# Kernel tuning notes

Measured on AMD Instinct MI355X. Metric: run time of the kernel, lower is better.

Reference implementation:

```python
import jax, jax.numpy as jnp
import numpy as np

B, S, H, K, L, NH, FF = 4, 2048, 2048, 1024, 2, 16, 4096
EPS = 1e-5

def _alibi_slopes(n):
    # standard power-of-two ALiBi slopes
    start = 2.0 ** (-8.0 / n)
    return start ** jnp.arange(1, n + 1, dtype=jnp.float32)

def _layernorm(h, g, b):
    mu = jnp.mean(h, axis=-1, keepdims=True)
    var = jnp.mean(jnp.square(h - mu), axis=-1, keepdims=True)
    return (h - mu) * jax.lax.rsqrt(var + EPS) * g + b

def setup_inputs() -> dict:
    key = jax.random.key(0)
    ks = jax.random.split(key, 16)
    x = jax.random.normal(ks[0], (B, S, H), jnp.float32)
    prev = jax.random.normal(ks[1], (B, S, H), jnp.float32)
    # unique sorted token indices per batch row (jit-friendly boolean mask)
    idx = jnp.stack([jnp.sort(jax.random.permutation(jax.random.fold_in(ks[2], b), S)[:K])
                     for b in range(B)]).astype(jnp.int32)
    w = 0.02
    Wq = jax.random.normal(ks[3], (L, H, H), jnp.float32) * w
    Wk = jax.random.normal(ks[4], (L, H, H), jnp.float32) * w
    Wv = jax.random.normal(ks[5], (L, H, H), jnp.float32) * w
    Wo = jax.random.normal(ks[6], (L, H, H), jnp.float32) * w
    attn_gamma = jnp.ones((L, H), jnp.float32)
    attn_beta = jnp.zeros((L, H), jnp.float32)
    mlp_gamma = jnp.ones((L, H), jnp.float32)
    mlp_beta = jnp.zeros((L, H), jnp.float32)
    Wgate = jax.random.normal(ks[7], (L, H, FF), jnp.float32) * w
    Wup = jax.random.normal(ks[8], (L, H, FF), jnp.float32) * w
    Wdown = jax.random.normal(ks[9], (L, FF, H), jnp.float32) * w
    return {"x": x, "prev": prev, "idx": idx, "Wq": Wq, "Wk": Wk, "Wv": Wv,
            "Wo": Wo, "attn_gamma": attn_gamma, "attn_beta": attn_beta,
            "mlp_gamma": mlp_gamma, "mlp_beta": mlp_beta,
            "Wgate": Wgate, "Wup": Wup, "Wdown": Wdown}

def _forward(x, prev, idx, Wq, Wk, Wv, Wo, attn_gamma, attn_beta,
             mlp_gamma, mlp_beta, Wgate, Wup, Wdown):
    d = H // NH
    scale = 1.0 / jnp.sqrt(jnp.asarray(d, jnp.float32))
    # gather selected tokens: [B, K, H]
    cur = jnp.take_along_axis(x, idx[:, :, None], axis=1)
    mem = jnp.take_along_axis(prev, idx[:, :, None], axis=1)
    # non-causal ALiBi bias over selected-sequence positions: [NH, K, K]
    pos = jnp.arange(K)
    dist = jnp.abs(pos[:, None] - pos[None, :]).astype(jnp.float32)
    bias = -_alibi_slopes(NH)[:, None, None] * dist
    for l in range(L):
        q = (cur @ Wq[l]).reshape(B, K, NH, d)
        k = (mem @ Wk[l]).reshape(B, K, NH, d)
        v = (mem @ Wv[l]).reshape(B, K, NH, d)
        scores = jnp.einsum('bqhd,bkhd->bhqk', q, k) * scale + bias
        attn = jax.nn.softmax(scores, axis=-1)
        o = jnp.einsum('bhqk,bkhd->bqhd', attn, v).reshape(B, K, H) @ Wo[l]
        cur = cur + o
        normed = _layernorm(cur, attn_gamma[l], attn_beta[l])
        mlp = (jax.nn.silu(normed @ Wgate[l]) * (normed @ Wup[l])) @ Wdown[l]
        cur = cur + mlp
        cur = _layernorm(cur, mlp_gamma[l], mlp_beta[l])
    # scatter-add back: out[mask] += update_val
    out = x.at[jnp.arange(B)[:, None], idx].add(cur)
    return out

def reference(x, prev, idx, Wq, Wk, Wv, Wo, attn_gamma, attn_beta,
              mlp_gamma, mlp_beta, Wgate, Wup, Wdown):
    return _forward(x, prev, idx, Wq, Wk, Wv, Wo, attn_gamma, attn_beta,
                    mlp_gamma, mlp_beta, Wgate, Wup, Wdown)
```

## Files before the change

### kernel.cpp

```cpp
#include <hip/hip_runtime.h>
#include <hip/hip_bf16.h>

#define BB 4
#define SS 2048
#define HH 2048
#define KK 1024
#define LL 2
#define NHH 16
#define FFF 4096
#define DD 128

typedef __attribute__((ext_vector_type(8))) short s8v;
typedef __attribute__((ext_vector_type(4))) short s4v;
typedef __attribute__((ext_vector_type(4))) float f4v;

__device__ __forceinline__ short f2bf(float f) {
  unsigned u = __builtin_bit_cast(unsigned, f);
  u += 0x7fffu + ((u >> 16) & 1u);
  return (short)(u >> 16);
}
__device__ __forceinline__ float bf2f(short s) {
  unsigned u = ((unsigned)(unsigned short)s) << 16;
  return __builtin_bit_cast(float, u);
}
__device__ __forceinline__ f4v mfma_bf16(s8v a, s8v b, f4v c) {
  asm("v_mfma_f32_16x16x32_bf16 %0, %1, %2, %0" : "+v"(c) : "v"(a), "v"(b));
  return c;
}
__device__ __forceinline__ void gload_lds16(const void* g, void* l) {
  __builtin_amdgcn_global_load_lds(
      (__attribute__((address_space(1))) void*)g,
      (__attribute__((address_space(3))) void*)l, 16, 0, 0);
}

__global__ __launch_bounds__(256) void wconv(const float* __restrict__ W,
                                             short* __restrict__ Wt,
                                             int Kd, int N) {
  __shared__ short tile[64][65];
  int n0 = blockIdx.x * 64, k0 = blockIdx.y * 64;
  int t = threadIdx.x;
#pragma unroll
  for (int i = 0; i < 16; ++i) {
    int lin = i * 256 + t;
    int r = lin >> 6, c = lin & 63;
    tile[c][r] = f2bf(W[(size_t)(k0 + r) * N + n0 + c]);
  }
  __syncthreads();
#pragma unroll
  for (int i = 0; i < 16; ++i) {
    int lin = i * 256 + t;
    int r = lin >> 6, c = lin & 63;
    Wt[(size_t)(n0 + r) * Kd + k0 + c] = tile[r][c];
  }
}

__global__ __launch_bounds__(256) void gather_rows(
    const float* __restrict__ x, const float* __restrict__ prev,
    const int* __restrict__ idx, float* __restrict__ cur_f,
    short* __restrict__ cur_b, short* __restrict__ mem_b) {
  int r = blockIdx.x;
  int b = r >> 10, kk = r & (KK - 1);
  int src = idx[b * KK + kk];
  const float4* xs = (const float4*)(x + ((size_t)b * SS + src) * HH);
  const float4* ps = (const float4*)(prev + ((size_t)b * SS + src) * HH);
  float4* cf = (float4*)(cur_f + (size_t)r * HH);
  s4v* cb = (s4v*)(cur_b + (size_t)r * HH);
  s4v* mb = (s4v*)(mem_b + (size_t)r * HH);
  int t = threadIdx.x;
#pragma unroll
  for (int i = 0; i < 2; ++i) {
    int c = t + i * 256;
    float4 xv = xs[c], pv = ps[c];
    cf[c] = xv;
    s4v cv, mv;
    cv[0] = f2bf(xv.x); cv[1] = f2bf(xv.y); cv[2] = f2bf(xv.z); cv[3] = f2bf(xv.w);
    mv[0] = f2bf(pv.x); mv[1] = f2bf(pv.y); mv[2] = f2bf(pv.z); mv[3] = f2bf(pv.w);
    cb[c] = cv; mb[c] = mv;
  }
}

template <int EPI>
__global__ __launch_bounds__(256, 2) void gemm_bt(
    const short* __restrict__ A, const short* __restrict__ Bt,
    float* __restrict__ Cf, short* __restrict__ Cb,
    const short* __restrict__ Other, int M, int N, int Kd) {
  __shared__ __align__(16) short As[128 * 32];
  __shared__ __align__(16) short Bs[128 * 32];
  int t = threadIdx.x;
  int w = t >> 6, l = t & 63;
  int wr = w >> 1, wc = w & 1;
  int l15 = l & 15, lh = l >> 4;
  int rowBase = blockIdx.y * 128, colBase = blockIdx.x * 128;

  f4v acc[4][4];
#pragma unroll
  for (int i = 0; i < 4; ++i)
#pragma unroll
    for (int j = 0; j < 4; ++j) acc[i][j] = (f4v){0.f, 0.f, 0.f, 0.f};

  int ar = t >> 2, ac = (t & 3) * 8;
  const short* gA = A + (size_t)(rowBase + ar) * Kd + ac;
  const short* gB = Bt + (size_t)(colBase + ar) * Kd + ac;
  short* lA = &As[t * 8];
  short* lB = &Bs[t * 8];
  int koff = lh * 8;

  for (int k0 = 0; k0 < Kd; k0 += 32) {
    gload_lds16(gA + k0, lA);
    gload_lds16(gA + k0 + (size_t)64 * Kd, lA + 2048);
    gload_lds16(gB + k0, lB);
    gload_lds16(gB + k0 + (size_t)64 * Kd, lB + 2048);
    __syncthreads();
    s8v af[4], bf[4];
#pragma unroll
    for (int mt = 0; mt < 4; ++mt)
      af[mt] = *(const s8v*)&As[(wr * 64 + mt * 16 + l15) * 32 + koff];
#pragma unroll
    for (int nt = 0; nt < 4; ++nt)
      bf[nt] = *(const s8v*)&Bs[(wc * 64 + nt * 16 + l15) * 32 + koff];
#pragma unroll
    for (int mt = 0; mt < 4; ++mt)
#pragma unroll
      for (int nt = 0; nt < 4; ++nt)
        acc[mt][nt] = mfma_bf16(af[mt], bf[nt], acc[mt][nt]);
    __syncthreads();
  }

#pragma unroll
  for (int mt = 0; mt < 4; ++mt) {
#pragma unroll
    for (int nt = 0; nt < 4; ++nt) {
#pragma unroll
      for (int r = 0; r < 4; ++r) {
        int row = rowBase + wr * 64 + mt * 16 + lh * 4 + r;
        int col = colBase + wc * 64 + nt * 16 + l15;
        float v = acc[mt][nt][r];
        if constexpr (EPI == 0) {
          Cb[(size_t)row * N + col] = f2bf(v);
        } else if constexpr (EPI == 1) {
          Cf[(size_t)row * N + col] += v;
        } else if constexpr (EPI == 2) {
          int b = row >> 10, ktok = row & (KK - 1);
          int h = col >> 7, dd = col & (DD - 1);
          Cb[(((size_t)(b * NHH + h)) * DD + dd) * KK + ktok] = f2bf(v);
        } else if constexpr (EPI == 3) {
          float sv = v / (1.f + __expf(-v));
          Cb[(size_t)row * N + col] = f2bf(sv);
        } else {
          float o = bf2f(Other[(size_t)row * N + col]);
          Cb[(size_t)row * N + col] = f2bf(v * o);
        }
      }
    }
  }
}

__global__ __launch_bounds__(256, 2) void attn_fwd(
    const short* __restrict__ qb, const short* __restrict__ kb,
    const short* __restrict__ vT, short* __restrict__ ob) {
  __shared__ __align__(16) short Kl[64 * 136];
  __shared__ __align__(16) short Vl[128 * 72];
  __shared__ __align__(16) short Pl[64 * 72];
  int b = blockIdx.z, h = blockIdx.y, qt = blockIdx.x;
  int t = threadIdx.x, w = t >> 6, l = t & 63, l15 = l & 15, lh = l >> 4;
  float slope = exp2f(-0.5f * (float)(h + 1));
  const float scale = 0.08838834764831845f;

  s8v qf[4];
  int qrowA = qt * 64 + w * 16 + l15;
  const short* qptr = qb + ((size_t)(b * KK + qrowA)) * HH + h * DD + lh * 8;
#pragma unroll
  for (int ks = 0; ks < 4; ++ks) qf[ks] = *(const s8v*)(qptr + ks * 32);

  f4v oacc[8];
#pragma unroll
  for (int i = 0; i < 8; ++i) oacc[i] = (f4v){0.f, 0.f, 0.f, 0.f};
  float m[4], sden[4];
#pragma unroll
  for (int r = 0; r < 4; ++r) { m[r] = -1e30f; sden[r] = 0.f; }
  int qpos_base = qt * 64 + w * 16 + lh * 4;

  for (int kt = 0; kt < KK / 64; ++kt) {
    {
      int rr = t >> 4, cc = (t & 15) * 8;
#pragma unroll
      for (int it = 0; it < 4; ++it) {
        int krow = it * 16 + rr;
        s8v g = *(const s8v*)(kb + ((size_t)(b * KK + kt * 64 + krow)) * HH + h * DD + cc);
        *(s8v*)&Kl[krow * 136 + cc] = g;
      }
      int dr = t >> 3, c2 = (t & 7) * 8;
#pragma unroll
      for (int it = 0; it < 4; ++it) {
        int drow = it * 32 + dr;
        s8v g = *(const s8v*)(vT + (((size_t)(b * NHH + h)) * DD + drow) * KK + kt * 64 + c2);
        *(s8v*)&Vl[drow * 72 + c2] = g;
      }
    }
    __syncthreads();

    f4v sacc[4];
#pragma unroll
    for (int ct = 0; ct < 4; ++ct) sacc[ct] = (f4v){0.f, 0.f, 0.f, 0.f};
#pragma unroll
    for (int ct = 0; ct < 4; ++ct)
#pragma unroll
      for (int ks = 0; ks < 4; ++ks) {
        s8v kf = *(const s8v*)&Kl[(ct * 16 + l15) * 136 + ks * 32 + lh * 8];
        sacc[ct] = mfma_bf16(qf[ks], kf, sacc[ct]);
      }

#pragma unroll
    for (int r = 0; r < 4; ++r) {
      int qpos = qpos_base + r;
      float mx = -1e30f;
#pragma unroll
      for (int ct = 0; ct < 4; ++ct) {
        int kpos = kt * 64 + ct * 16 + l15;
        float sv = sacc[ct][r] * scale - slope * fabsf((float)(qpos - kpos));
        sacc[ct][r] = sv;
        mx = fmaxf(mx, sv);
      }
      mx = fmaxf(mx, __shfl_xor(mx, 1));
      mx = fmaxf(mx, __shfl_xor(mx, 2));
      mx = fmaxf(mx, __shfl_xor(mx, 4));
      mx = fmaxf(mx, __shfl_xor(mx, 8));
      float mn = fmaxf(m[r], mx);
      float corr = __expf(m[r] - mn);
      m[r] = mn;
      float ps = 0.f;
#pragma unroll
      for (int ct = 0; ct < 4; ++ct) {
        float p = __expf(sacc[ct][r] - mn);
        sacc[ct][r] = p;
        ps += p;
      }
      ps += __shfl_xor(ps, 1); ps += __shfl_xor(ps, 2);
      ps += __shfl_xor(ps, 4); ps += __shfl_xor(ps, 8);
      sden[r] = sden[r] * corr + ps;
#pragma unroll
      for (int dt = 0; dt < 8; ++dt) oacc[dt][r] *= corr;
#pragma unroll
      for (int ct = 0; ct < 4; ++ct)
        Pl[(w * 16 + lh * 4 + r) * 72 + ct * 16 + l15] = f2bf(sacc[ct][r]);
    }

#pragma unroll
    for (int ks2 = 0; ks2 < 2; ++ks2) {
      s8v pa = *(const s8v*)&Pl[(w * 16 + l15) * 72 + ks2 * 32 + lh * 8];
#pragma unroll
      for (int dt = 0; dt < 8; ++dt) {
        s8v vf = *(const s8v*)&Vl[(dt * 16 + l15) * 72 + ks2 * 32 + lh * 8];
        oacc[dt] = mfma_bf16(pa, vf, oacc[dt]);
      }
    }
    __syncthreads();
  }

#pragma unroll
  for (int dt = 0; dt < 8; ++dt)
#pragma unroll
    for (int r = 0; r < 4; ++r) {
      int qpos = qpos_base + r;
      int dd = dt * 16 + l15;
      ob[((size_t)(b * KK + qpos)) * HH + h * DD + dd] = f2bf(oacc[dt][r] / sden[r]);
    }
}

__global__ __launch_bounds__(256) void ln_rows(const float* in,
    const float* __restrict__ gma, const float* __restrict__ bta,
    short* __restrict__ outb, float* outf) {
  __shared__ float red[2][4];
  int r = blockIdx.x, t = threadIdx.x;
  const float4* x4 = (const float4*)(in + (size_t)r * HH);
  float4 va = x4[t], vb = x4[t + 256];
  float sum = va.x + va.y + va.z + va.w + vb.x + vb.y + vb.z + vb.w;
  float sq = va.x * va.x + va.y * va.y + va.z * va.z + va.w * va.w +
             vb.x * vb.x + vb.y * vb.y + vb.z * vb.z + vb.w * vb.w;
#pragma unroll
  for (int off = 32; off; off >>= 1) {
    sum += __shfl_down(sum, off);
    sq += __shfl_down(sq, off);
  }
  int w = t >> 6;
  if ((t & 63) == 0) { red[0][w] = sum; red[1][w] = sq; }
  __syncthreads();
  sum = red[0][0] + red[0][1] + red[0][2] + red[0][3];
  sq = red[1][0] + red[1][1] + red[1][2] + red[1][3];
  float mu = sum * (1.f / HH);
  float rs = rsqrtf(sq * (1.f / HH) - mu * mu + 1e-5f);
  const float4* g4 = (const float4*)gma;
  const float4* b4 = (const float4*)bta;
  s4v* ob = (s4v*)(outb + (size_t)r * HH);
  float4* of = (float4*)(outf ? outf + (size_t)r * HH : nullptr);
#pragma unroll
  for (int i = 0; i < 2; ++i) {
    int c = t + i * 256;
    float4 v = (i == 0) ? va : vb;
    float4 g = g4[c], bb = b4[c];
    float4 nv;
    nv.x = (v.x - mu) * rs * g.x + bb.x;
    nv.y = (v.y - mu) * rs * g.y + bb.y;
    nv.z = (v.z - mu) * rs * g.z + bb.z;
    nv.w = (v.w - mu) * rs * g.w + bb.w;
    s4v o;
    o[0] = f2bf(nv.x); o[1] = f2bf(nv.y); o[2] = f2bf(nv.z); o[3] = f2bf(nv.w);
    ob[c] = o;
    if (outf) of[c] = nv;
  }
}

__global__ __launch_bounds__(256) void copy_out(const float* __restrict__ x,
                                                float* __restrict__ out, size_t n4) {
  size_t i = (size_t)blockIdx.x * 256 + threadIdx.x;
  size_t stride = (size_t)gridDim.x * 256;
  const float4* xi = (const float4*)x;
  float4* oi = (float4*)out;
  for (; i < n4; i += stride) oi[i] = xi[i];
}

__global__ __launch_bounds__(256) void scatter_add(const int* __restrict__ idx,
                                                   const float* __restrict__ cur,
                                                   float* out) {
  int r = blockIdx.x;
  int b = r >> 10, kk = r & (KK - 1);
  int dst = idx[b * KK + kk];
  float4* o = (float4*)(out + ((size_t)b * SS + dst) * HH);
  const float4* c = (const float4*)(cur + (size_t)r * HH);
  int t = threadIdx.x;
#pragma unroll
  for (int i = 0; i < 2; ++i) {
    int j = t + i * 256;
    float4 ov = o[j], cv = c[j];
    ov.x += cv.x; ov.y += cv.y; ov.z += cv.z; ov.w += cv.w;
    o[j] = ov;
  }
}

extern "C" void kernel_launch(void* const* d_in, const int* in_sizes, int n_in,
                              void* d_out, int out_size, void* d_ws, size_t ws_size,
                              hipStream_t stream) {
  (void)in_sizes; (void)n_in; (void)out_size; (void)ws_size;
  const float* x = (const float*)d_in[0];
  const float* prv = (const float*)d_in[1];
  const int* idx = (const int*)d_in[2];
  const float* Wq = (const float*)d_in[3];
  const float* Wk = (const float*)d_in[4];
  const float* Wv = (const float*)d_in[5];
  const float* Wo = (const float*)d_in[6];
  const float* ag = (const float*)d_in[7];
  const float* ab = (const float*)d_in[8];
  const float* mg = (const float*)d_in[9];
  const float* mbt = (const float*)d_in[10];
  const float* Wg = (const float*)d_in[11];
  const float* Wu = (const float*)d_in[12];
  const float* Wd = (const float*)d_in[13];
  float* out = (float*)d_out;

  char* ws = (char*)d_ws;
  size_t off = 0;
  auto alloc = [&](size_t bytes) -> void* {
    void* p = ws + off;
    off += (bytes + 255) & ~(size_t)255;
    return p;
  };
  const size_t WHH = (size_t)HH * HH, WHF = (size_t)HH * FFF;
  short* WqT = (short*)alloc(LL * WHH * 2);
  short* WkT = (short*)alloc(LL * WHH * 2);
  short* WvT = (short*)alloc(LL * WHH * 2);
  short* WoT = (short*)alloc(LL * WHH * 2);
  short* WgT = (short*)alloc(LL * WHF * 2);
  short* WuT = (short*)alloc(LL * WHF * 2);
  short* WdT = (short*)alloc(LL * WHF * 2);
  const size_t RH = (size_t)BB * KK * HH;
  float* cur_f = (float*)alloc(RH * 4);
  short* q_b = (short*)alloc(RH * 2);
  short* k_b = (short*)alloc(RH * 2);
  short* vT_b = (short*)alloc(RH * 2);
  short* o_b = (short*)alloc(RH * 2);
  short* cur_b = (short*)alloc(RH * 2);
  short* mem_b = (short*)alloc(RH * 2);
  short* nrm_b = (short*)alloc(RH * 2);
  short* sg_b = q_b;
  short* hid_b = vT_b;

  dim3 blk(256);
  for (int l = 0; l < LL; ++l) {
    wconv<<<dim3(HH / 64, HH / 64), blk, 0, stream>>>(Wq + l * WHH, WqT + l * WHH, HH, HH);
    wconv<<<dim3(HH / 64, HH / 64), blk, 0, stream>>>(Wk + l * WHH, WkT + l * WHH, HH, HH);
    wconv<<<dim3(HH / 64, HH / 64), blk, 0, stream>>>(Wv + l * WHH, WvT + l * WHH, HH, HH);
    wconv<<<dim3(HH / 64, HH / 64), blk, 0, stream>>>(Wo + l * WHH, WoT + l * WHH, HH, HH);
    wconv<<<dim3(FFF / 64, HH / 64), blk, 0, stream>>>(Wg + l * WHF, WgT + l * WHF, HH, FFF);
    wconv<<<dim3(FFF / 64, HH / 64), blk, 0, stream>>>(Wu + l * WHF, WuT + l * WHF, HH, FFF);
    wconv<<<dim3(HH / 64, FFF / 64), blk, 0, stream>>>(Wd + l * WHF, WdT + l * WHF, FFF, HH);
  }
  gather_rows<<<dim3(BB * KK), blk, 0, stream>>>(x, prv, idx, cur_f, cur_b, mem_b);

  const int M = BB * KK;
  for (int l = 0; l < LL; ++l) {
    const short* wq = WqT + l * WHH;
    const short* wk = WkT + l * WHH;
    const short* wv = WvT + l * WHH;
    const short* wo = WoT + l * WHH;
    const short* wg = WgT + l * WHF;
    const short* wu = WuT + l * WHF;
    const short* wd = WdT + l * WHF;
    gemm_bt<0><<<dim3(HH / 128, M / 128), blk, 0, stream>>>(cur_b, wq, nullptr, q_b, nullptr, M, HH, HH);
    gemm_bt<0><<<dim3(HH / 128, M / 128), blk, 0, stream>>>(mem_b, wk, nullptr, k_b, nullptr, M, HH, HH);
    gemm_bt<2><<<dim3(HH / 128, M / 128), blk, 0, stream>>>(mem_b, wv, nullptr, vT_b, nullptr, M, HH, HH);
    attn_fwd<<<dim3(KK / 64, NHH, BB), blk, 0, stream>>>(q_b, k_b, vT_b, o_b);
    gemm_bt<1><<<dim3(HH / 128, M / 128), blk, 0, stream>>>(o_b, wo, cur_f, nullptr, nullptr, M, HH, HH);
    ln_rows<<<dim3(M), blk, 0, stream>>>(cur_f, ag + l * HH, ab + l * HH, nrm_b, nullptr);
    gemm_bt<3><<<dim3(FFF / 128, M / 128), blk, 0, stream>>>(nrm_b, wg, nullptr, sg_b, nullptr, M, FFF, HH);
    gemm_bt<4><<<dim3(FFF / 128, M / 128), blk, 0, stream>>>(nrm_b, wu, nullptr, hid_b, sg_b, M, FFF, HH);
    gemm_bt<1><<<dim3(HH / 128, M / 128), blk, 0, stream>>>(hid_b, wd, cur_f, nullptr, nullptr, M, HH, FFF);
    ln_rows<<<dim3(M), blk, 0, stream>>>(cur_f, mg + l * HH, mbt + l * HH, cur_b, cur_f);
  }
  copy_out<<<dim3(2048), blk, 0, stream>>>(x, out, (size_t)BB * SS * HH / 4);
  scatter_add<<<dim3(M), blk, 0, stream>>>(idx, cur_f, out);
}
```

Before: 1.464 ms.

## Double-buffer GEMM LDS tiles with 512-thread 128x256 blocks and swizzled block order

Replaces the 256-thread 128x128 GEMM with a 512-thread kernel computing 128x256 tiles. LDS is double-buffered so the next K-slice loads while MFMAs run on the current one, leaving one barrier per iteration instead of two. Block IDs are remapped across 8 groups, likely to spread or localise work across XCDs for cache reuse. The remap assumes gridDim.y is a power of two and the block count is divisible by 8, and the larger LDS footprint may limit occupancy.

```diff
diff --git a/kernel.cpp b/kernel.cpp
--- a/kernel.cpp
+++ b/kernel.cpp
@@ -23,7 +23,7 @@
   unsigned u = ((unsigned)(unsigned short)s) << 16;
   return __builtin_bit_cast(float, u);
 }
-__device__ __forceinline__ f4v mfma_bf16(s8v a, s8v b, f4v c) {
+__device__ __forceinline__ f4v mfma16(s8v a, s8v b, f4v c) {
   asm("v_mfma_f32_16x16x32_bf16 %0, %1, %2, %0" : "+v"(c) : "v"(a), "v"(b));
   return c;
 }
@@ -80,17 +80,31 @@
 }
 
 template <int EPI>
-__global__ __launch_bounds__(256, 2) void gemm_bt(
+__global__ __launch_bounds__(512, 2) void g8p(
     const short* __restrict__ A, const short* __restrict__ Bt,
     float* __restrict__ Cf, short* __restrict__ Cb,
     const short* __restrict__ Other, int M, int N, int Kd) {
-  __shared__ __align__(16) short As[128 * 32];
-  __shared__ __align__(16) short Bs[128 * 32];
-  int t = threadIdx.x;
-  int w = t >> 6, l = t & 63;
-  int wr = w >> 1, wc = w & 1;
-  int l15 = l & 15, lh = l >> 4;
-  int rowBase = blockIdx.y * 128, colBase = blockIdx.x * 128;
+  __shared__ __align__(16) short smem[2 * 12288];
+  const int t = threadIdx.x;
+  const int w = t >> 6, l = t & 63;
+  const int wr = w >> 2, wc = w & 3;
+  const int l15 = l & 15, lh = l >> 4;
+  const int koff = lh * 8;
+
+  const int gx = gridDim.x, gy = gridDim.y;
+  const int nwg = gx * gy;
+  const int bid = blockIdx.y * gx + blockIdx.x;
+  const int wg = (bid & 7) * (nwg >> 3) + (bid >> 3);
+  const int by = wg & (gy - 1);
+  const int bx = wg / gy;
+  const int rowBase = by * 128, colBase = bx * 256;
+
+  const int ar = t >> 2, ac = (t & 3) * 8;
+  const short* gA = A + (size_t)(rowBase + ar) * Kd + ac;
+  const short* gB0 = Bt + (size_t)(colBase + ar) * Kd + ac;
+  const short* gB1 = gB0 + (size_t)128 * Kd;
+  short* lA = smem + t * 8;
+  short* lB = smem + 4096 + t * 8;
 
   f4v acc[4][4];
 #pragma unroll
@@ -98,32 +112,34 @@
 #pragma unroll
     for (int j = 0; j < 4; ++j) acc[i][j] = (f4v){0.f, 0.f, 0.f, 0.f};
 
-  int ar = t >> 2, ac = (t & 3) * 8;
-  const short* gA = A + (size_t)(rowBase + ar) * Kd + ac;
-  const short* gB = Bt + (size_t)(colBase + ar) * Kd + ac;
-  short* lA = &As[t * 8];
-  short* lB = &Bs[t * 8];
-  int koff = lh * 8;
-
-  for (int k0 = 0; k0 < Kd; k0 += 32) {
-    gload_lds16(gA + k0, lA);
-    gload_lds16(gA + k0 + (size_t)64 * Kd, lA + 2048);
-    gload_lds16(gB + k0, lB);
-    gload_lds16(gB + k0 + (size_t)64 * Kd, lB + 2048);
+  const int NT = Kd >> 5;
+  gload_lds16(gA, lA);
+  gload_lds16(gB0, lB);
+  gload_lds16(gB1, lB + 4096);
+  __syncthreads();
+
+  for (int kt = 0; kt < NT; ++kt) {
+    const short* sb = smem + (kt & 1) * 12288;
+    if (kt + 1 < NT) {
+      const int k0 = (kt + 1) * 32;
+      const int o = ((kt & 1) ^ 1) * 12288;
+      gload_lds16(gA + k0, lA + o);
+      gload_lds16(gB0 + k0, lB + o);
+      gload_lds16(gB1 + k0, lB + o + 4096);
+    }
+    s8v af[4], bf[4];
+#pragma unroll
+    for (int mt = 0; mt < 4; ++mt)
+      af[mt] = *(const s8v*)(sb + (wr * 64 + mt * 16 + l15) * 32 + koff);
+#pragma unroll
+    for (int nt = 0; nt < 4; ++nt)
+      bf[nt] = *(const s8v*)(sb + 4096 + (wc * 64 + nt * 16 + l15) * 32 + koff);
+#pragma unroll
+    for (int mt = 0; mt < 4; ++mt)
+#pragma unroll
+      for (int nt = 0; nt < 4; ++nt)
+        acc[mt][nt] = mfma16(af[mt], bf[nt], acc[mt][nt]);
     __syncthreads();
-    s8v af[4], bf[4];
-#pragma unroll
-    for (int mt = 0; mt < 4; ++mt)
-      af[mt] = *(const s8v*)&As[(wr * 64 + mt * 16 + l15) * 32 + koff];
-#pragma unroll
-    for (int nt = 0; nt < 4; ++nt)
-      bf[nt] = *(const s8v*)&Bs[(wc * 64 + nt * 16 + l15) * 32 + koff];
-#pragma unroll
-    for (int mt = 0; mt < 4; ++mt)
-#pragma unroll
-      for (int nt = 0; nt < 4; ++nt)
-        acc[mt][nt] = mfma_bf16(af[mt], bf[nt], acc[mt][nt]);
-    __syncthreads();
   }
 
 #pragma unroll
@@ -131,10 +147,10 @@
 #pragma unroll
     for (int nt = 0; nt < 4; ++nt) {
 #pragma unroll
-      for (int r = 0; r < 4; ++r) {
-        int row = rowBase + wr * 64 + mt * 16 + lh * 4 + r;
+      for (int rr = 0; rr < 4; ++rr) {
+        int row = rowBase + wr * 64 + mt * 16 + lh * 4 + rr;
         int col = colBase + wc * 64 + nt * 16 + l15;
-        float v = acc[mt][nt][r];
+        float v = acc[mt][nt][rr];
         if constexpr (EPI == 0) {
           Cb[(size_t)row * N + col] = f2bf(v);
         } else if constexpr (EPI == 1) {
@@ -207,7 +223,7 @@
 #pragma unroll
       for (int ks = 0; ks < 4; ++ks) {
         s8v kf = *(const s8v*)&Kl[(ct * 16 + l15) * 136 + ks * 32 + lh * 8];
-        sacc[ct] = mfma_bf16(qf[ks], kf, sacc[ct]);
+        sacc[ct] = mfma16(qf[ks], kf, sacc[ct]);
       }
 
 #pragma unroll
@@ -251,7 +267,7 @@
 #pragma unroll
       for (int dt = 0; dt < 8; ++dt) {
         s8v vf = *(const s8v*)&Vl[(dt * 16 + l15) * 72 + ks2 * 32 + lh * 8];
-        oacc[dt] = mfma_bf16(pa, vf, oacc[dt]);
+        oacc[dt] = mfma16(pa, vf, oacc[dt]);
       }
     }
     __syncthreads();
@@ -384,7 +400,7 @@
   short* sg_b = q_b;
   short* hid_b = vT_b;
 
-  dim3 blk(256);
+  dim3 blk(256), blk512(512);
   for (int l = 0; l < LL; ++l) {
     wconv<<<dim3(HH / 64, HH / 64), blk, 0, stream>>>(Wq + l * WHH, WqT + l * WHH, HH, HH);
     wconv<<<dim3(HH / 64, HH / 64), blk, 0, stream>>>(Wk + l * WHH, WkT + l * WHH, HH, HH);
@@ -402,18 +418,18 @@
     const short* wk = WkT + l * WHH;
     const short* wv = WvT + l * WHH;
     const short* wo = WoT + l * WHH;
-    const short* wg = WgT + l * WHF;
+    const short* wg_ = WgT + l * WHF;
     const short* wu = WuT + l * WHF;
     const short* wd = WdT + l * WHF;
-    gemm_bt<0><<<dim3(HH / 128, M / 128), blk, 0, stream>>>(cur_b, wq, nullptr, q_b, nullptr, M, HH, HH);
-    gemm_bt<0><<<dim3(HH / 128, M / 128), blk, 0, stream>>>(mem_b, wk, nullptr, k_b, nullptr, M, HH, HH);
-    gemm_bt<2><<<dim3(HH / 128, M / 128), blk, 0, stream>>>(mem_b, wv, nullptr, vT_b, nullptr, M, HH, HH);
+    g8p<0><<<dim3(HH / 256, M / 128), blk512, 0, stream>>>(cur_b, wq, nullptr, q_b, nullptr, M, HH, HH);
+    g8p<0><<<dim3(HH / 256, M / 128), blk512, 0, stream>>>(mem_b, wk, nullptr, k_b, nullptr, M, HH, HH);
+    g8p<2><<<dim3(HH / 256, M / 128), blk512, 0, stream>>>(mem_b, wv, nullptr, vT_b, nullptr, M, HH, HH);
     attn_fwd<<<dim3(KK / 64, NHH, BB), blk, 0, stream>>>(q_b, k_b, vT_b, o_b);
-    gemm_bt<1><<<dim3(HH / 128, M / 128), blk, 0, stream>>>(o_b, wo, cur_f, nullptr, nullptr, M, HH, HH);
+    g8p<1><<<dim3(HH / 256, M / 128), blk512, 0, stream>>>(o_b, wo, cur_f, nullptr, nullptr, M, HH, HH);
     ln_rows<<<dim3(M), blk, 0, stream>>>(cur_f, ag + l * HH, ab + l * HH, nrm_b, nullptr);
-    gemm_bt<3><<<dim3(FFF / 128, M / 128), blk, 0, stream>>>(nrm_b, wg, nullptr, sg_b, nullptr, M, FFF, HH);
-    gemm_bt<4><<<dim3(FFF / 128, M / 128), blk, 0, stream>>>(nrm_b, wu, nullptr, hid_b, sg_b, M, FFF, HH);
-    gemm_bt<1><<<dim3(HH / 128, M / 128), blk, 0, stream>>>(hid_b, wd, cur_f, nullptr, nullptr, M, HH, FFF);
+    g8p<3><<<dim3(FFF / 256, M / 128), blk512, 0, stream>>>(nrm_b, wg_, nullptr, sg_b, nullptr, M, FFF, HH);
+    g8p<4><<<dim3(FFF / 256, M / 128), blk512, 0, stream>>>(nrm_b, wu, nullptr, hid_b, sg_b, M, FFF, HH);
+    g8p<1><<<dim3(HH / 256, M / 128), blk512, 0, stream>>>(hid_b, wd, cur_f, nullptr, nullptr, M, HH, FFF);
     ln_rows<<<dim3(M), blk, 0, stream>>>(cur_f, mg + l * HH, mbt + l * HH, cur_b, cur_f);
   }
   copy_out<<<dim3(2048), blk, 0, stream>>>(x, out, (size_t)BB * SS * HH / 4);
```

Measured after the change: 1.447 ms. Within noise of the previous version (-1.2%).
